# Kernel tuning notes

Measured on AMD Instinct MI355X. Metric: run time of the kernel, lower is better.

## Reference

```python
import jax, jax.numpy as jnp
import numpy as np

ALPHA = 0.5
GAMMA = 0.01
TOP_K = 5
B, T, C = 2048, 8192, 1  # C must be 1 for amp_loss's grouped conv1d to be valid


def _ashift_loss(inp, tgt):
    _, t_len, _ = inp.shape
    sm = jax.nn.softmax(inp - tgt, axis=1)                      # [B,T,C]
    return jnp.mean(jnp.sum(jnp.abs(1.0 / t_len - sm), axis=1, keepdims=True))


def _phase_loss(inp, tgt, top_k=TOP_K):
    inp_f = jnp.fft.rfft(inp, axis=1)                           # [B,Tf,C] complex
    tgt_f = jnp.fft.rfft(tgt, axis=1)
    b, tf_len, c = tgt_f.shape
    amp = jnp.abs(tgt_f).at[:, 0, :].set(0.0)                   # zero DC bin
    # top-k magnitudes along freq axis (per batch, per channel)
    _, idx = jax.lax.top_k(jnp.transpose(amp, (0, 2, 1)), top_k)  # [B,C,k]
    top = jnp.transpose(idx, (0, 2, 1))                         # [B,k,C]
    # boolean mask: True everywhere except top-k freq bins (per column)
    freqs = jnp.arange(tf_len)
    mask = ~jnp.any(freqs[None, :, None, None] == top[:, None, :, :], axis=2)  # [B,Tf,C]
    # replicate torch row-major boolean-mask flatten + view(B, Tf-k, C):
    flat = mask.reshape(b, tf_len * c)
    order = jnp.argsort(~flat, axis=1, stable=True)             # kept (True) positions first, in row-major order
    keep = order[:, : (tf_len - top_k) * c]                     # flat (t*C + c') positions
    non_top = (keep // c).reshape(b, tf_len - top_k, c)         # stored value is the freq index t
    dom = jnp.take_along_axis(tgt_f, top, axis=1) - jnp.take_along_axis(inp_f, top, axis=1)
    domain_loss = jnp.mean(jnp.sqrt(jnp.sum(jnp.abs(dom) ** 2, axis=1)))
    gath = jnp.take_along_axis(inp_f, non_top, axis=1)          # [B,Tf-k,C]
    nondomain_loss = jnp.mean(jnp.sqrt(jnp.sum(jnp.abs(gath) ** 2, axis=1, keepdims=True)))
    return domain_loss + nondomain_loss


def _amp_loss(inp, tgt):
    # Valid only for C==1: conv1d([B,1,T], weight=[B,1,T], groups=1) -> [B,B,1]
    # out[b,o] = sum_t tgt[b,t] * flip(kernel)[o,t]
    t2 = tgt[:, :, 0]                                           # [B,T]
    i2 = inp[:, :, 0]
    flip_diff = t2[:, ::-1] - i2[:, ::-1]                       # flip(target) - flip(input)
    diff = jnp.einsum('bt,ot->bo', t2, flip_diff)               # self_corr - cross_corr, [B,B]
    # torch.norm(p=2) over the singleton dim == abs
    return jnp.mean(jnp.abs(diff))


def setup_inputs() -> dict:
    key = jax.random.key(0)
    k1, k2 = jax.random.split(key)
    inp = jax.random.normal(k1, (B, T, C), dtype=jnp.float32)
    tgt = jax.random.normal(k2, (B, T, C), dtype=jnp.float32)
    return {"input": inp, "target": tgt}


def reference(input, target):
    return (ALPHA * _ashift_loss(input, target)
            + (1.0 - ALPHA) * _phase_loss(input, target)
            + GAMMA * _amp_loss(input, target))
```

## Files before the change

kernel.cpp:

```cpp
#include <hip/hip_runtime.h>
#include <hip/hip_bf16.h>
#include <math.h>

#define B_N 2048
#define T_N 8192
#define NFFT 4096
#define TF_LEN 4097
#define TOPK 5
#define KSPLIT 4
#define GBK 64

#define ZIDX(n) ((n) + ((n) >> 4))
#define ZPAD (NFFT + (NFFT >> 4))

typedef float f32x4 __attribute__((ext_vector_type(4)));
typedef __bf16 bf16x8 __attribute__((ext_vector_type(8)));
typedef unsigned short ushort_t;

__device__ __forceinline__ void gload_lds16(const ushort_t* g, ushort_t* l) {
    __builtin_amdgcn_global_load_lds(
        (const __attribute__((address_space(1))) void*)g,
        (__attribute__((address_space(3))) void*)l,
        16, 0, 0);
}

__device__ __forceinline__ float wave_reduce_sum(float v) {
    for (int o = 32; o >= 1; o >>= 1) v += __shfl_xor(v, o, 64);
    return v;
}
__device__ __forceinline__ float wave_reduce_max(float v) {
    for (int o = 32; o >= 1; o >>= 1) v = fmaxf(v, __shfl_xor(v, o, 64));
    return v;
}

__device__ __forceinline__ ushort_t f2bf(float x) {
    __hip_bfloat16 h = __float2bfloat16(x);
    return *reinterpret_cast<ushort_t*>(&h);
}

__device__ __forceinline__ float2 cis_rev(float rev) {
    return make_float2(__builtin_amdgcn_cosf(rev), __builtin_amdgcn_sinf(rev));
}
__device__ __forceinline__ float2 cmulf(float2 a, float2 b) {
    return make_float2(a.x * b.x - a.y * b.y, a.x * b.y + a.y * b.x);
}

__global__ __launch_bounds__(256) void init_kernel(float* acc, float* Cpart, int nzbuf) {
    if (blockIdx.x == 0 && threadIdx.x < 4) acc[threadIdx.x] = 0.0f;
    if (nzbuf == 1) {
        size_t idx = ((size_t)blockIdx.x * 256 + threadIdx.x) * 4;
        *reinterpret_cast<f32x4*>(&Cpart[idx]) = (f32x4){0.f, 0.f, 0.f, 0.f};
    }
}

__device__ __forceinline__ void dft4(float2 x0, float2 x1, float2 x2, float2 x3,
                                     float2* y0, float2* y1, float2* y2, float2* y3) {
    float2 t0 = make_float2(x0.x + x2.x, x0.y + x2.y);
    float2 t1 = make_float2(x0.x - x2.x, x0.y - x2.y);
    float2 t2 = make_float2(x1.x + x3.x, x1.y + x3.y);
    float2 t3 = make_float2(x1.x - x3.x, x1.y - x3.y);
    *y0 = make_float2(t0.x + t2.x, t0.y + t2.y);
    *y2 = make_float2(t0.x - t2.x, t0.y - t2.y);
    *y1 = make_float2(t1.x + t3.y, t1.y - t3.x);
    *y3 = make_float2(t1.x - t3.y, t1.y + t3.x);
}

__device__ __forceinline__ void dft16(float2 X[16]) {
    float2 G[16];
    dft4(X[0], X[4], X[8],  X[12], &G[0],  &G[1],  &G[2],  &G[3]);
    dft4(X[1], X[5], X[9],  X[13], &G[4],  &G[5],  &G[6],  &G[7]);
    dft4(X[2], X[6], X[10], X[14], &G[8],  &G[9],  &G[10], &G[11]);
    dft4(X[3], X[7], X[11], X[15], &G[12], &G[13], &G[14], &G[15]);
    const float C1 = 0.9238795325112867f, S1 = 0.3826834323650898f;
    const float R2 = 0.7071067811865476f;
    G[5]  = cmulf(G[5],  make_float2(C1, -S1));
    G[6]  = cmulf(G[6],  make_float2(R2, -R2));
    G[7]  = cmulf(G[7],  make_float2(S1, -C1));
    G[9]  = cmulf(G[9],  make_float2(R2, -R2));
    { float2 g = G[10]; G[10] = make_float2(g.y, -g.x); }
    G[11] = cmulf(G[11], make_float2(-R2, -R2));
    G[13] = cmulf(G[13], make_float2(S1, -C1));
    G[14] = cmulf(G[14], make_float2(-R2, -R2));
    G[15] = cmulf(G[15], make_float2(-C1, S1));
    dft4(G[0], G[4], G[8],  G[12], &X[0], &X[4], &X[8],  &X[12]);
    dft4(G[1], G[5], G[9],  G[13], &X[1], &X[5], &X[9],  &X[13]);
    dft4(G[2], G[6], G[10], G[14], &X[2], &X[6], &X[10], &X[14]);
    dft4(G[3], G[7], G[11], G[15], &X[3], &X[7], &X[11], &X[15]);
}

__device__ __forceinline__ void rfft_bin(const float2* Zs, int k, float* orr, float* oi) {
    int kk = k & (NFFT - 1);
    int nk = (NFFT - k) & (NFFT - 1);
    float2 zk = Zs[ZIDX(kk)], znk = Zs[ZIDX(nk)];
    float xer = 0.5f * (zk.x + znk.x);
    float xei = 0.5f * (zk.y - znk.y);
    float xo_r = 0.5f * (zk.y + znk.y);
    float xo_i = -0.5f * (zk.x - znk.x);
    float2 w = cis_rev((float)k * (-1.0f / (float)T_N));
    *orr = xer + w.x * xo_r - w.y * xo_i;
    *oi = xei + w.x * xo_i + w.y * xo_r;
}

__global__ __launch_bounds__(256) void fused_row_kernel(const float* __restrict__ inp,
                                                        const float* __restrict__ tgt,
                                                        ushort_t* __restrict__ Abf,
                                                        ushort_t* __restrict__ Bbf,
                                                        float* acc) {
    __shared__ float2 Zs[ZPAD];
    __shared__ float red[4];
    __shared__ float wv[2][4];
    __shared__ int wi[2][4];
    __shared__ float2 tgtF[TOPK];
    __shared__ float rscratch[64];

    int b = blockIdx.x;
    int tid = threadIdx.x;
    int lane = tid & 63, wid = tid >> 6;
    const float* tp = tgt + (size_t)b * T_N;
    const float* ip = inp + (size_t)b * T_N;
    ushort_t* Ab = Abf + (size_t)b * T_N;
    ushort_t* Bb = Bbf + (size_t)b * T_N;

    float4 trv[8];
#pragma unroll
    for (int i = 0; i < 8; i++) {
        int q = tid + 256 * i;
        trv[i] = *reinterpret_cast<const float4*>(&tp[4 * q]);
        ushort4 ua;
        ua.x = f2bf(trv[i].x); ua.y = f2bf(trv[i].y);
        ua.z = f2bf(trv[i].z); ua.w = f2bf(trv[i].w);
        *reinterpret_cast<ushort4*>(&Ab[4 * q]) = ua;
        int m0 = 2 * q, m1 = 2 * q + 1;
        int p0 = ((m0 & 15) << 8) | (m0 & 0x0F0) | (m0 >> 8);
        int p1 = ((m1 & 15) << 8) | (m1 & 0x0F0) | (m1 >> 8);
        Zs[ZIDX(p0)] = make_float2(trv[i].x, trv[i].y);
        Zs[ZIDX(p1)] = make_float2(trv[i].z, trv[i].w);
    }

    float4 irv[8], dv[8];
#pragma unroll
    for (int i = 0; i < 8; i++) {
        int q = tid + 256 * i;
        irv[i] = *reinterpret_cast<const float4*>(&ip[4 * q]);
        dv[i] = make_float4(irv[i].x - trv[i].x, irv[i].y - trv[i].y,
                            irv[i].z - trv[i].z, irv[i].w - trv[i].w);
        ushort4 ub;
        ub.x = f2bf(-dv[i].w); ub.y = f2bf(-dv[i].z);
        ub.z = f2bf(-dv[i].y); ub.w = f2bf(-dv[i].x);
        uint2 p = *reinterpret_cast<uint2*>(&ub);
        p.x = __shfl_xor(p.x, 63, 64);
        p.y = __shfl_xor(p.y, 63, 64);
        int o = lane + 64 * (31 - wid - 4 * i);
        *reinterpret_cast<uint2*>(&Bb[4 * o]) = p;
    }

    {
        float lmax = -1e30f;
#pragma unroll
        for (int i = 0; i < 8; i++)
            lmax = fmaxf(lmax, fmaxf(fmaxf(dv[i].x, dv[i].y), fmaxf(dv[i].z, dv[i].w)));
        lmax = wave_reduce_max(lmax);
        if (lane == 0) red[wid] = lmax;
        __syncthreads();
        float mx = fmaxf(fmaxf(red[0], red[1]), fmaxf(red[2], red[3]));
        __syncthreads();
        float lsum = 0.0f;
#pragma unroll
        for (int i = 0; i < 8; i++) {
            dv[i].x = __expf(dv[i].x - mx);
            dv[i].y = __expf(dv[i].y - mx);
            dv[i].z = __expf(dv[i].z - mx);
            dv[i].w = __expf(dv[i].w - mx);
            lsum += (dv[i].x + dv[i].y) + (dv[i].z + dv[i].w);
        }
        lsum = wave_reduce_sum(lsum);
        if (lane == 0) red[wid] = lsum;
        __syncthreads();
        float Z = (red[0] + red[1]) + (red[2] + red[3]);
        __syncthreads();
        float inv = 1.0f / Z;
        const float u = 1.0f / (float)T_N;
        float labs = 0.0f;
#pragma unroll
        for (int i = 0; i < 8; i++) {
            labs += fabsf(u - dv[i].x * inv) + fabsf(u - dv[i].y * inv) +
                    fabsf(u - dv[i].z * inv) + fabsf(u - dv[i].w * inv);
        }
        labs = wave_reduce_sum(labs);
        if (lane == 0) red[wid] = labs;
        __syncthreads();
        if (tid == 0)
            atomicAdd(acc + 0, (red[0] + red[1]) + (red[2] + red[3]));
    }
    __syncthreads();

    {
        float2 X[16];
        int base = tid * 16;
#pragma unroll
        for (int r = 0; r < 16; r++) X[r] = Zs[ZIDX(base + r)];
        dft16(X);
#pragma unroll
        for (int r = 0; r < 16; r++) Zs[ZIDX(base + r)] = X[r];
    }
    __syncthreads();
    {
        float2 X[16];
        int j = tid & 15;
        int base = (tid >> 4) * 256 + j;
#pragma unroll
        for (int r = 0; r < 16; r++) X[r] = Zs[ZIDX(base + 16 * r)];
        float2 w1 = cis_rev(-(float)j * (1.0f / 256.0f));
        float2 w = w1;
#pragma unroll
        for (int r = 1; r < 16; r++) { X[r] = cmulf(X[r], w); w = cmulf(w, w1); }
        dft16(X);
#pragma unroll
        for (int r = 0; r < 16; r++) Zs[ZIDX(base + 16 * r)] = X[r];
    }
    __syncthreads();
    {
        float2 X[16];
#pragma unroll
        for (int r = 0; r < 16; r++) X[r] = Zs[ZIDX(tid + 256 * r)];
        float2 w1 = cis_rev(-(float)tid * (1.0f / 4096.0f));
        float2 w = w1;
#pragma unroll
        for (int r = 1; r < 16; r++) { X[r] = cmulf(X[r], w); w = cmulf(w, w1); }
        dft16(X);
#pragma unroll
        for (int r = 0; r < 16; r++) Zs[ZIDX(tid + 256 * r)] = X[r];
    }
    __syncthreads();

    float av[16];
    float aN = -3.0f;
    {
        float2 rot = cis_rev(-(float)tid * (1.0f / (float)T_N));
        const float2 drot = make_float2(0.9807852804032304f, -0.19509032201612825f);
#pragma unroll
        for (int i = 0; i < 16; i++) {
            int k = tid + 256 * i;
            if (i == 0 && tid == 0) {
                av[i] = -1.0f;
            } else {
                int nk = (NFFT - k) & (NFFT - 1);
                float2 zk = Zs[ZIDX(k & (NFFT - 1))], znk = Zs[ZIDX(nk)];
                float xer = 0.5f * (zk.x + znk.x);
                float xei = 0.5f * (zk.y - znk.y);
                float xo_r = 0.5f * (zk.y + znk.y);
                float xo_i = -0.5f * (zk.x - znk.x);
                float xr = xer + rot.x * xo_r - rot.y * xo_i;
                float xi = xei + rot.x * xo_i + rot.y * xo_r;
                av[i] = xr * xr + xi * xi;
            }
            rot = cmulf(rot, drot);
        }
        if (tid == 0) {
            float2 z0 = Zs[ZIDX(0)];
            float v = z0.x - z0.y;
            aN = v * v;
        }
    }

    int fqa[TOPK];
#pragma unroll
    for (int r = 0; r < TOPK; r++) {
        float bv = -3.0f;
        int bi = TF_LEN;
#pragma unroll
        for (int i = 0; i < 16; i++) {
            float a = av[i];
            if (a > bv) { bv = a; bi = tid + 256 * i; }
        }
        if (aN > bv) { bv = aN; bi = 4096; }
        for (int o = 1; o < 64; o <<= 1) {
            float ov = __shfl_xor(bv, o, 64);
            int oi = __shfl_xor(bi, o, 64);
            if (ov > bv || (ov == bv && oi < bi)) { bv = ov; bi = oi; }
        }
        if (lane == 0) { wv[r & 1][wid] = bv; wi[r & 1][wid] = bi; }
        __syncthreads();
        float fv = wv[r & 1][0];
        int fi = wi[r & 1][0];
#pragma unroll
        for (int w2 = 1; w2 < 4; w2++) {
            float cv = wv[r & 1][w2];
            int ci = wi[r & 1][w2];
            if (cv > fv || (cv == fv && ci < fi)) { fv = cv; fi = ci; }
        }
        fqa[r] = fi;
        if (fi == 4096) {
            if (tid == 0) aN = -2.0f;
        } else if ((fi & 255) == tid) {
            int slot = fi >> 8;
#pragma unroll
            for (int i = 0; i < 16; i++)
                if (i == slot) av[i] = -2.0f;
        }
    }

    if (tid < TOPK) {
        int myf = fqa[0];
        if (tid == 1) myf = fqa[1];
        if (tid == 2) myf = fqa[2];
        if (tid == 3) myf = fqa[3];
        if (tid == 4) myf = fqa[4];
        float xr, xi;
        rfft_bin(Zs, myf, &xr, &xi);
        tgtF[tid] = make_float2(xr, xi);
    }
    __syncthreads();

    float2 cur[TOPK], wr[TOPK];
    float pre[TOPK][4], pim[TOPK][4];
#pragma unroll
    for (int q = 0; q < TOPK; q++) {
        int f = fqa[q];
        cur[q] = cis_rev(-(float)((f * 4 * tid) & (T_N - 1)) * (1.0f / (float)T_N));
        wr[q] = cis_rev(-(float)((f * 1024) & (T_N - 1)) * (1.0f / (float)T_N));
#pragma unroll
        for (int c = 0; c < 4; c++) { pre[q][c] = 0.0f; pim[q][c] = 0.0f; }
    }
    float E = 0.0f, sev = 0.0f, sod = 0.0f;
#pragma unroll
    for (int i = 0; i < 8; i++) {
        float4 v = irv[i];
        E = fmaf(v.x, v.x, E); sev += v.x;
        E = fmaf(v.y, v.y, E); sod += v.y;
        E = fmaf(v.z, v.z, E); sev += v.z;
        E = fmaf(v.w, v.w, E); sod += v.w;
#pragma unroll
        for (int q = 0; q < TOPK; q++) {
            pre[q][0] = fmaf(v.x, cur[q].x, pre[q][0]);
            pim[q][0] = fmaf(v.x, cur[q].y, pim[q][0]);
            pre[q][1] = fmaf(v.y, cur[q].x, pre[q][1]);
            pim[q][1] = fmaf(v.y, cur[q].y, pim[q][1]);
            pre[q][2] = fmaf(v.z, cur[q].x, pre[q][2]);
            pim[q][2] = fmaf(v.z, cur[q].y, pim[q][2]);
            pre[q][3] = fmaf(v.w, cur[q].x, pre[q][3]);
            pim[q][3] = fmaf(v.w, cur[q].y, pim[q][3]);
            cur[q] = cmulf(cur[q], wr[q]);
        }
    }
    float re[TOPK], im[TOPK];
#pragma unroll
    for (int q = 0; q < TOPK; q++) {
        float2 wcq = cis_rev(-(float)fqa[q] * (1.0f / (float)T_N));
        float tr = pre[q][3], ti = pim[q][3];
        float ur = pre[q][2] + (wcq.x * tr - wcq.y * ti);
        float ui = pim[q][2] + (wcq.x * ti + wcq.y * tr);
        float vr = pre[q][1] + (wcq.x * ur - wcq.y * ui);
        float vi = pim[q][1] + (wcq.x * ui + wcq.y * ur);
        re[q] = pre[q][0] + (wcq.x * vr - wcq.y * vi);
        im[q] = pim[q][0] + (wcq.x * vi + wcq.y * vr);
    }

    float vals[13] = {re[0], im[0], re[1], im[1], re[2], im[2], re[3], im[3],
                      re[4], im[4], E, sev + sod, sev - sod};
#pragma unroll
    for (int i = 0; i < 13; i++) {
        float v = wave_reduce_sum(vals[i]);
        if (lane == 0) rscratch[wid * 13 + i] = v;
    }
    __syncthreads();
    if (tid == 0) {
        float tot[13];
        for (int i = 0; i < 13; i++)
            tot[i] = rscratch[i] + rscratch[13 + i] + rscratch[26 + i] + rscratch[39 + i];
        float dsum = 0, isum = 0;
        for (int q = 0; q < TOPK; q++) {
            float rr = tot[2 * q], ii = tot[2 * q + 1];
            float dr = tgtF[q].x - rr, di = tgtF[q].y - ii;
            dsum += dr * dr + di * di;
            isum += rr * rr + ii * ii;
        }
        float Ee = tot[10], X0v = tot[11], Xhv = tot[12];
        float S_all = 0.5f * ((float)T_N * Ee + X0v * X0v + Xhv * Xhv);
        float val = sqrtf(dsum) + sqrtf(fmaxf(S_all - isum, 0.0f));
        atomicAdd(acc + 1, val);
    }
}

__global__ __launch_bounds__(512, 2) void gemm_kernel(const ushort_t* __restrict__ A,
                                                      const ushort_t* __restrict__ Bm,
                                                      float* __restrict__ Cpart,
                                                      int nzbuf) {
    __shared__ __align__(16) ushort_t lds[2][4][128 * 64];
    int tid = threadIdx.x;
    int bid = blockIdx.x;
    int swz = ((bid & 7) << 5) | (bid >> 3);
    int bx = swz & 7, by = (swz >> 3) & 7, bz = swz >> 6;
    int row0 = bx * 256, col0 = by * 256;
    const int KC = T_N / KSPLIT;
    const int NT = KC / GBK;
    const int NIT = NT / 2;
    int kbase = bz * KC;

    int w = tid >> 6, lane = tid & 63;
    int wm = w >> 2, wn = w & 3;
    int lr = lane & 15, kq = lane >> 4;

    f32x4 accf[8][4];
#pragma unroll
    for (int mi = 0; mi < 8; mi++)
#pragma unroll
        for (int ni = 0; ni < 4; ni++) accf[mi][ni] = (f32x4){0.f, 0.f, 0.f, 0.f};

    int strow = tid >> 3;
    int scb = (tid & 7) ^ (strow & 7);
    const ushort_t* gA0 = A + (size_t)(row0 + strow) * T_N + kbase + scb * 8;
    const ushort_t* gA1 = A + (size_t)(row0 + 128 + strow) * T_N + kbase + scb * 8;
    const ushort_t* gB0 = Bm + (size_t)(col0 + strow) * T_N + kbase + scb * 8;
    const ushort_t* gB1 = Bm + (size_t)(col0 + 128 + strow) * T_N + kbase + scb * 8;
    const size_t SUB = (size_t)64 * T_N;

    int rb0 = lr * 64 + ((kq ^ (lr & 7)) << 3);
    int rb1 = lr * 64 + (((4 + kq) ^ (lr & 7)) << 3);

#define SA_(s, buf, kt)                                                        \
    do {                                                                       \
        gload_lds16(gA0 + (s) * SUB + (size_t)(kt) * GBK, &lds[buf][0][(s) * 4096 + tid * 8]); \
        gload_lds16(gA1 + (s) * SUB + (size_t)(kt) * GBK, &lds[buf][1][(s) * 4096 + tid * 8]); \
    } while (0)
#define SB_(rg, buf, kt)                                                       \
    do {                                                                       \
        const ushort_t* g_ = ((rg) == 2) ? gB0 : gB1;                          \
        gload_lds16(g_ + (size_t)(kt) * GBK, &lds[buf][rg][tid * 8]);          \
        gload_lds16(g_ + SUB + (size_t)(kt) * GBK, &lds[buf][rg][4096 + tid * 8]); \
    } while (0)

#define PHASE(BUF, QM, QN, VMN, STAGE_STMT)                                    \
    do {                                                                       \
        asm volatile("s_waitcnt vmcnt(" #VMN ")" ::: "memory");                \
        const ushort_t* Ab_ = &lds[BUF][wm][0];                                \
        const ushort_t* Bb_ = &lds[BUF][2 + (wn >> 1)][(wn & 1) * 4096];       \
        bf16x8 a_[4][2], b_[2][2];                                             \
        _Pragma("unroll") for (int m_ = 0; m_ < 4; m_++) {                     \
            a_[m_][0] = *reinterpret_cast<const bf16x8*>(Ab_ + (QM) * 4096 + m_ * 1024 + rb0); \
            a_[m_][1] = *reinterpret_cast<const bf16x8*>(Ab_ + (QM) * 4096 + m_ * 1024 + rb1); \
        }                                                                      \
        _Pragma("unroll") for (int n_ = 0; n_ < 2; n_++) {                     \
            b_[n_][0] = *reinterpret_cast<const bf16x8*>(Bb_ + (QN) * 2048 + n_ * 1024 + rb0); \
            b_[n_][1] = *reinterpret_cast<const bf16x8*>(Bb_ + (QN) * 2048 + n_ * 1024 + rb1); \
        }                                                                      \
        STAGE_STMT;                                                            \
        __builtin_amdgcn_s_barrier();                                          \
        __builtin_amdgcn_s_setprio(1);                                         \
        _Pragma("unroll") for (int m_ = 0; m_ < 4; m_++)                       \
        _Pragma("unroll") for (int n_ = 0; n_ < 2; n_++) {                     \
            accf[(QM) * 4 + m_][(QN) * 2 + n_] = __builtin_amdgcn_mfma_f32_16x16x32_bf16( \
                a_[m_][0], b_[n_][0], accf[(QM) * 4 + m_][(QN) * 2 + n_], 0, 0, 0); \
            accf[(QM) * 4 + m_][(QN) * 2 + n_] = __builtin_amdgcn_mfma_f32_16x16x32_bf16( \
                a_[m_][1], b_[n_][1], accf[(QM) * 4 + m_][(QN) * 2 + n_], 0, 0, 0); \
        }                                                                      \
        __builtin_amdgcn_s_setprio(0);                                         \
        __builtin_amdgcn_s_barrier();                                          \
    } while (0)

    SA_(0, 0, 0);
    SA_(1, 0, 0);
    SB_(2, 0, 0);
    SB_(3, 0, 0);
    SA_(0, 1, 1);
    asm volatile("s_waitcnt vmcnt(2)" ::: "memory");
    __builtin_amdgcn_s_barrier();

    for (int it = 0; it < NIT; ++it) {
        int kt1 = 2 * it + 1;
        int te = (2 * it + 2 < NT) ? 2 * it + 2 : 2 * it;
        int to = (kt1 + 2 < NT) ? kt1 + 2 : kt1;
        PHASE(0, 0, 0, 4, SB_(3, 1, kt1));
        PHASE(0, 0, 1, 4, SB_(2, 1, kt1));
        PHASE(0, 1, 0, 6, SA_(0, 0, te));
        PHASE(0, 1, 1, 2, SA_(1, 1, kt1));
        PHASE(1, 0, 0, 4, SB_(3, 0, te));
        PHASE(1, 0, 1, 2, SB_(2, 0, te));
        PHASE(1, 1, 0, 4, SA_(1, 0, te));
        PHASE(1, 1, 1, 2, SA_(0, 1, to));
    }
#undef PHASE
#undef SA_
#undef SB_

    int crow = row0 + wm * 128 + (lane >> 4) * 4;
    int ccol = col0 + wn * 64 + lr;
    if (nzbuf == 4) {
        float* Cp = Cpart + (size_t)bz * ((size_t)B_N * B_N);
#pragma unroll
        for (int mi = 0; mi < 8; mi++)
#pragma unroll
            for (int ni = 0; ni < 4; ni++)
#pragma unroll
                for (int r = 0; r < 4; r++)
                    Cp[(size_t)(crow + mi * 16 + r) * B_N + ccol + ni * 16] =
                        accf[mi][ni][r];
    } else {
#pragma unroll
        for (int mi = 0; mi < 8; mi++)
#pragma unroll
            for (int ni = 0; ni < 4; ni++)
#pragma unroll
                for (int r = 0; r < 4; r++)
                    atomicAdd(&Cpart[(size_t)(crow + mi * 16 + r) * B_N + ccol + ni * 16],
                              accf[mi][ni][r]);
    }
}

__global__ __launch_bounds__(256) void absum_kernel(const float* __restrict__ C,
                                                    float* acc, int nzbuf) {
    __shared__ float sred[4];
    int tid = threadIdx.x;
    int lane = tid & 63, wid = tid >> 6;
    const size_t NN = (size_t)B_N * B_N;
    size_t base = (size_t)blockIdx.x * 4096;
    float s = 0.0f;
#pragma unroll
    for (int i = 0; i < 4; i++) {
        size_t idx = base + (size_t)(tid + 256 * i) * 4;
        f32x4 v = *reinterpret_cast<const f32x4*>(&C[idx]);
        if (nzbuf == 4) {
            v += *reinterpret_cast<const f32x4*>(&C[NN + idx]);
            v += *reinterpret_cast<const f32x4*>(&C[2 * NN + idx]);
            v += *reinterpret_cast<const f32x4*>(&C[3 * NN + idx]);
        }
        s += fabsf(v.x) + fabsf(v.y) + fabsf(v.z) + fabsf(v.w);
    }
    s = wave_reduce_sum(s);
    if (lane == 0) sred[wid] = s;
    __syncthreads();
    if (tid == 0) atomicAdd(acc + 2, sred[0] + sred[1] + sred[2] + sred[3]);
}

__global__ void combine_kernel(const float* acc, float* out) {
    if (threadIdx.x == 0) {
        float ash = acc[0] / (float)B_N;
        float ph = acc[1] / (float)B_N;
        float am = acc[2] / ((float)B_N * (float)B_N);
        out[0] = 0.5f * ash + 0.5f * ph + 0.01f * am;
    }
}

extern "C" void kernel_launch(void* const* d_in, const int* in_sizes, int n_in,
                              void* d_out, int out_size, void* d_ws, size_t ws_size,
                              hipStream_t stream) {
    const float* inp = (const float*)d_in[0];
    const float* tgt = (const float*)d_in[1];
    float* acc = (float*)d_ws;
    ushort_t* Abf = (ushort_t*)((char*)d_ws + 256);
    ushort_t* Bbf = Abf + (size_t)B_N * T_N;
    float* Cpart = (float*)(Bbf + (size_t)B_N * T_N);
    float* out = (float*)d_out;

    size_t need4 = 256 + 2 * (size_t)B_N * T_N * sizeof(ushort_t)
                 + (size_t)KSPLIT * (size_t)B_N * B_N * sizeof(float);
    int nzbuf = (ws_size >= need4) ? 4 : 1;

    hipLaunchKernelGGL(init_kernel, dim3(nzbuf == 1 ? 4096 : 1), dim3(256), 0, stream,
                       acc, Cpart, nzbuf);
    hipLaunchKernelGGL(fused_row_kernel, dim3(B_N), dim3(256), 0, stream,
                       inp, tgt, Abf, Bbf, acc);
    hipLaunchKernelGGL(gemm_kernel, dim3(256), dim3(512), 0, stream,
                       Abf, Bbf, Cpart, nzbuf);
    hipLaunchKernelGGL(absum_kernel, dim3(1024), dim3(256), 0, stream,
                       Cpart, acc, nzbuf);
    hipLaunchKernelGGL(combine_kernel, dim3(1), dim3(1), 0, stream, acc, out);
}
```

Before: 180.5 us.

## Repad FFT LDS layout, use power-tree twiddles, and trim softmax barriers

```diff
diff --git a/kernel.cpp b/kernel.cpp
--- a/kernel.cpp
+++ b/kernel.cpp
@@ -10,8 +10,8 @@
 #define KSPLIT 4
 #define GBK 64
 
-#define ZIDX(n) ((n) + ((n) >> 4))
-#define ZPAD (NFFT + (NFFT >> 4))
+#define ZIDX(n) ((n) + ((n) >> 4) + ((n) >> 8))
+#define ZPAD (NFFT + (NFFT >> 4) + (NFFT >> 8))
 
 typedef float f32x4 __attribute__((ext_vector_type(4)));
 typedef __bf16 bf16x8 __attribute__((ext_vector_type(8)));
@@ -43,6 +43,24 @@
 }
 __device__ __forceinline__ float2 cmulf(float2 a, float2 b) {
     return make_float2(a.x * b.x - a.y * b.y, a.x * b.y + a.y * b.x);
+}
+
+__device__ __forceinline__ void gen_pows(float2 w1, float2 tw[16]) {
+    tw[1] = w1;
+    tw[2] = cmulf(w1, w1);
+    tw[3] = cmulf(tw[2], w1);
+    tw[4] = cmulf(tw[2], tw[2]);
+    tw[5] = cmulf(tw[4], w1);
+    tw[6] = cmulf(tw[4], tw[2]);
+    tw[7] = cmulf(tw[4], tw[3]);
+    tw[8] = cmulf(tw[4], tw[4]);
+    tw[9] = cmulf(tw[8], w1);
+    tw[10] = cmulf(tw[8], tw[2]);
+    tw[11] = cmulf(tw[8], tw[3]);
+    tw[12] = cmulf(tw[8], tw[4]);
+    tw[13] = cmulf(tw[8], tw[5]);
+    tw[14] = cmulf(tw[8], tw[6]);
+    tw[15] = cmulf(tw[8], tw[7]);
 }
 
 __global__ __launch_bounds__(256) void init_kernel(float* acc, float* Cpart, int nzbuf) {
@@ -107,7 +125,7 @@
                                                         ushort_t* __restrict__ Bbf,
                                                         float* acc) {
     __shared__ float2 Zs[ZPAD];
-    __shared__ float red[4];
+    __shared__ float red[12];
     __shared__ float wv[2][4];
     __shared__ int wi[2][4];
     __shared__ float2 tgtF[TOPK];
@@ -163,7 +181,6 @@
         if (lane == 0) red[wid] = lmax;
         __syncthreads();
         float mx = fmaxf(fmaxf(red[0], red[1]), fmaxf(red[2], red[3]));
-        __syncthreads();
         float lsum = 0.0f;
 #pragma unroll
         for (int i = 0; i < 8; i++) {
@@ -174,10 +191,9 @@
             lsum += (dv[i].x + dv[i].y) + (dv[i].z + dv[i].w);
         }
         lsum = wave_reduce_sum(lsum);
-        if (lane == 0) red[wid] = lsum;
+        if (lane == 0) red[4 + wid] = lsum;
         __syncthreads();
-        float Z = (red[0] + red[1]) + (red[2] + red[3]);
-        __syncthreads();
+        float Z = (red[4] + red[5]) + (red[6] + red[7]);
         float inv = 1.0f / Z;
         const float u = 1.0f / (float)T_N;
         float labs = 0.0f;
@@ -187,12 +203,11 @@
                     fabsf(u - dv[i].z * inv) + fabsf(u - dv[i].w * inv);
         }
         labs = wave_reduce_sum(labs);
-        if (lane == 0) red[wid] = labs;
+        if (lane == 0) red[8 + wid] = labs;
         __syncthreads();
         if (tid == 0)
-            atomicAdd(acc + 0, (red[0] + red[1]) + (red[2] + red[3]));
-    }
-    __syncthreads();
+            atomicAdd(acc + 0, (red[8] + red[9]) + (red[10] + red[11]));
+    }
 
     {
         float2 X[16];
@@ -210,10 +225,10 @@
         int base = (tid >> 4) * 256 + j;
 #pragma unroll
         for (int r = 0; r < 16; r++) X[r] = Zs[ZIDX(base + 16 * r)];
-        float2 w1 = cis_rev(-(float)j * (1.0f / 256.0f));
-        float2 w = w1;
-#pragma unroll
-        for (int r = 1; r < 16; r++) { X[r] = cmulf(X[r], w); w = cmulf(w, w1); }
+        float2 tw[16];
+        gen_pows(cis_rev(-(float)j * (1.0f / 256.0f)), tw);
+#pragma unroll
+        for (int r = 1; r < 16; r++) X[r] = cmulf(X[r], tw[r]);
         dft16(X);
 #pragma unroll
         for (int r = 0; r < 16; r++) Zs[ZIDX(base + 16 * r)] = X[r];
@@ -223,10 +238,10 @@
         float2 X[16];
 #pragma unroll
         for (int r = 0; r < 16; r++) X[r] = Zs[ZIDX(tid + 256 * r)];
-        float2 w1 = cis_rev(-(float)tid * (1.0f / 4096.0f));
-        float2 w = w1;
-#pragma unroll
-        for (int r = 1; r < 16; r++) { X[r] = cmulf(X[r], w); w = cmulf(w, w1); }
+        float2 tw[16];
+        gen_pows(cis_rev(-(float)tid * (1.0f / 4096.0f)), tw);
+#pragma unroll
+        for (int r = 1; r < 16; r++) X[r] = cmulf(X[r], tw[r]);
         dft16(X);
 #pragma unroll
         for (int r = 0; r < 16; r++) Zs[ZIDX(tid + 256 * r)] = X[r];
@@ -236,14 +251,26 @@
     float av[16];
     float aN = -3.0f;
     {
-        float2 rot = cis_rev(-(float)tid * (1.0f / (float)T_N));
-        const float2 drot = make_float2(0.9807852804032304f, -0.19509032201612825f);
+        const float CC[16] = {
+            1.0f, 0.9807852804032304f, 0.9238795325112867f, 0.8314696123025452f,
+            0.7071067811865476f, 0.5555702330196022f, 0.3826834323650898f,
+            0.1950903220161283f, 0.0f, -0.1950903220161283f, -0.3826834323650898f,
+            -0.5555702330196022f, -0.7071067811865476f, -0.8314696123025452f,
+            -0.9238795325112867f, -0.9807852804032304f};
+        const float SS[16] = {
+            0.0f, -0.1950903220161283f, -0.3826834323650898f, -0.5555702330196022f,
+            -0.7071067811865476f, -0.8314696123025452f, -0.9238795325112867f,
+            -0.9807852804032304f, -1.0f, -0.9807852804032304f, -0.9238795325112867f,
+            -0.8314696123025452f, -0.7071067811865476f, -0.5555702330196022f,
+            -0.3826834323650898f, -0.1950903220161283f};
+        float2 rot0 = cis_rev(-(float)tid * (1.0f / (float)T_N));
 #pragma unroll
         for (int i = 0; i < 16; i++) {
             int k = tid + 256 * i;
             if (i == 0 && tid == 0) {
                 av[i] = -1.0f;
             } else {
+                float2 rot = cmulf(rot0, make_float2(CC[i], SS[i]));
                 int nk = (NFFT - k) & (NFFT - 1);
                 float2 zk = Zs[ZIDX(k & (NFFT - 1))], znk = Zs[ZIDX(nk)];
                 float xer = 0.5f * (zk.x + znk.x);
@@ -254,7 +281,6 @@
                 float xi = xei + rot.x * xo_i + rot.y * xo_r;
                 av[i] = xr * xr + xi * xi;
             }
-            rot = cmulf(rot, drot);
         }
         if (tid == 0) {
             float2 z0 = Zs[ZIDX(0)];
```

Result: no change. 179.2 us, median of 3 (-0.7%).
